# Kernel tuning notes

Hardware: AMD Instinct MI355X
Metric: run time of the kernel (lower is better)

Reference implementation:

```python
import jax, jax.numpy as jnp
import numpy as np

# ---- static config (mirrors init_kwargs) ----
WIN_X, WIN_Y = 12, 12
GRID_X, GRID_Y = 468, 468
BATCH = 4
SHIFTS = ((0, 0), (6, 6))
MAX_WIN_X = GRID_X // WIN_X + 1            # 40
MAX_WIN_Y = GRID_Y // WIN_Y + 1            # 40
MAX_WIN_PER_SAMPLE = MAX_WIN_X * MAX_WIN_Y # 1600
# (level, max_tokens, drop_range_lo, drop_range_hi)
DROP_INFO = ((0, 30, 0, 30), (1, 60, 30, 60), (2, 100, 60, 100000))
SENTINEL = 2_000_000_000  # window id for masked-out voxels (sorts to the end)


def _window_partition(coors):
    # coors: [N,4] = [b, z, y, x] int32 -> batch-unique window index per shift
    out = []
    for sx, sy in SHIFTS:
        x = coors[:, 3] + sx
        y = coors[:, 2] + sy
        wx = x // WIN_X
        wy = y // WIN_Y
        out.append((coors[:, 0] * MAX_WIN_PER_SAMPLE + wx * MAX_WIN_Y + wy).astype(jnp.int32))
    return out


def _sort_group_stats(win):
    # inner index within each equal-value group (counting-sort style) and group size per element
    order = jnp.argsort(win)                      # stable
    s = win[order]
    n = win.shape[0]
    left_s = jnp.searchsorted(s, s, side='left')
    inner_sorted = jnp.arange(n, dtype=win.dtype) - left_s.astype(win.dtype)
    inner = jnp.zeros_like(win).at[order].set(inner_sorted)
    counts = (jnp.searchsorted(s, win, side='right') - jnp.searchsorted(s, win, side='left')).astype(win.dtype)
    return inner, counts


def _drop_single_shift(win, valid):
    # equivalent of SSTInputLayer.drop_single_shift restricted to `valid` voxels
    w = jnp.where(valid, win, SENTINEL)
    inner, counts = _sort_group_stats(w)
    target = jnp.zeros_like(w)
    lvl = -jnp.ones_like(w)
    for dl, max_tok, lo, hi in DROP_INFO:
        m = (counts >= lo) & (counts < hi)
        target = jnp.where(m, max_tok, target)
        lvl = jnp.where(m, dl, lvl)
    keep = valid & (inner < target)
    return keep, jnp.where(valid, lvl, -1)


def _make_continuous(w):
    # dense-rank of window ids (make_continuous_inds) over a sentinel-masked array
    order = jnp.argsort(w)
    s = w[order]
    new_grp = jnp.concatenate([jnp.zeros((1,), w.dtype), (s[1:] != s[:-1]).astype(w.dtype)])
    rank = jnp.cumsum(new_grp)
    return jnp.zeros_like(w).at[order].set(rank)


def _flat2win(win, keep, lvl):
    # per-voxel position in the [num_windows, max_tokens] buffer of its drop level; -1 if dropped
    out = -jnp.ones_like(win)
    for dl, max_tok, _, _ in DROP_INFO:
        valid = keep & (lvl == dl)
        w = jnp.where(valid, win, SENTINEL)
        conti = _make_continuous(w)
        inner, _ = _sort_group_stats(w)
        out = jnp.where(valid, conti * max_tok + inner, out)
    return out


def reference(voxel_feat, coors):
    coors = coors.astype(jnp.int32)
    bwi0, bwi1 = _window_partition(coors)
    n = voxel_feat.shape[0]
    all_valid = jnp.ones((n,), bool)
    keep0, lvl0 = _drop_single_shift(bwi0, all_valid)
    keep1, lvl1 = _drop_single_shift(bwi1, keep0)   # shift-1 drop computed among shift-0 survivors
    keep = keep0 & keep1
    feat = jnp.where(keep[:, None], voxel_feat, 0.0)  # fixed-shape analogue of voxel_feat[voxel_keep_inds]
    f2w0 = _flat2win(bwi0, keep, lvl0)
    f2w1 = _flat2win(bwi1, keep, lvl1)
    return feat, keep, lvl0, lvl1, bwi0, bwi1, f2w0, f2w1


def setup_inputs() -> dict:
    key = jax.random.key(0)
    k1, k2, k3, k4 = jax.random.split(key, 4)
    n, c = 300000, 128
    voxel_feat = jax.random.normal(k1, (n, c), dtype=jnp.float32)
    b = jax.random.randint(k2, (n,), 0, BATCH)
    y = jax.random.randint(k3, (n,), 0, GRID_Y)
    x = jax.random.randint(k4, (n,), 0, GRID_X)
    z = jnp.zeros((n,), jnp.int32)
    coors = jnp.stack([b, z, y, x], axis=1).astype(jnp.int32)
    return {"voxel_feat": voxel_feat, "coors": coors}
```

## Files before the change

### kernel.cpp

```cpp
#include <hip/hip_runtime.h>


#define NWIN 6400
#define SEG_CAP 3072

__global__ void k_zero(int* __restrict__ hdr, int* __restrict__ keepF, int n) {
    int i = blockIdx.x * blockDim.x + threadIdx.x;
    if (i < 4 * NWIN) hdr[i] = 0;
    if (i < n) keepF[i] = 0;
}

__global__ void k_windows(const int* __restrict__ coors, int n,
                          int* __restrict__ w0a, int* __restrict__ w1a,
                          int* __restrict__ cnt0) {
    int i = blockIdx.x * blockDim.x + threadIdx.x;
    if (i >= n) return;
    int b = coors[4 * i];
    int y = coors[4 * i + 2];
    int x = coors[4 * i + 3];
    int w0 = b * 1600 + (x / 12) * 40 + (y / 12);
    int w1 = b * 1600 + ((x + 6) / 12) * 40 + ((y + 6) / 12);
    w0a[i] = w0;
    w1a[i] = w1;
    atomicAdd(&cnt0[w0], 1);
}

__global__ void k_scan(const int* __restrict__ cnt, int* __restrict__ base,
                       int* __restrict__ lvlW) {
    __shared__ int psum[256];
    int t = threadIdx.x;
    int st = t * 25;
    int s = 0;
    for (int j = 0; j < 25; j++) s += cnt[st + j];
    psum[t] = s;
    __syncthreads();
    if (t == 0) {
        int acc = 0;
        for (int j = 0; j < 256; j++) { int v = psum[j]; psum[j] = acc; acc += v; }
    }
    __syncthreads();
    int acc = psum[t];
    for (int j = 0; j < 25; j++) {
        int w = st + j;
        int c = cnt[w];
        base[w] = acc;
        acc += c;
        int lvl;
        if (c < 30) lvl = 0;
        else if (c < 60) lvl = 1;
        else if (c < 100000) lvl = 2;
        else lvl = -1;
        lvlW[w] = lvl;
    }
}

__global__ void k_count_masked(const int* __restrict__ wa, const int* __restrict__ mask,
                               int n, int* __restrict__ cnt) {
    int i = blockIdx.x * blockDim.x + threadIdx.x;
    if (i >= n) return;
    if (!mask[i]) return;
    atomicAdd(&cnt[wa[i]], 1);
}

__global__ void k_scatter(const int* __restrict__ wa, const int* __restrict__ mask, int n,
                          const int* __restrict__ base, int* __restrict__ cur,
                          int* __restrict__ seg) {
    int i = blockIdx.x * blockDim.x + threadIdx.x;
    if (i >= n) return;
    if (mask && !mask[i]) return;
    int w = wa[i];
    int p = atomicAdd(&cur[w], 1);
    seg[base[w] + p] = i;
}

__global__ void k_rankkeep(const int* __restrict__ cnt, const int* __restrict__ base,
                           const int* __restrict__ seg, int* __restrict__ keepOut) {
    int w = blockIdx.x;
    int k = cnt[w];
    if (k == 0) return;
    int bs = base[w];
    int target;
    if (k < 30) target = 30;
    else if (k < 60) target = 60;
    else if (k < 100000) target = 100;
    else target = 0;
    __shared__ int lds[SEG_CAP];
    if (k <= SEG_CAP) {
        for (int j = threadIdx.x; j < k; j += blockDim.x) lds[j] = seg[bs + j];
        __syncthreads();
        for (int e = threadIdx.x; e < k; e += blockDim.x) {
            int v = lds[e];
            int r = 0;
            for (int j = 0; j < k; j++) r += (lds[j] < v) ? 1 : 0;
            keepOut[v] = (r < target) ? 1 : 0;
        }
    } else {
        for (int e = threadIdx.x; e < k; e += blockDim.x) {
            int v = seg[bs + e];
            int r = 0;
            for (int j = 0; j < k; j++) r += (seg[bs + j] < v) ? 1 : 0;
            keepOut[v] = (r < target) ? 1 : 0;
        }
    }
}

__global__ void k_rankkept(const int* __restrict__ cnt, const int* __restrict__ base,
                           const int* __restrict__ seg, const int* __restrict__ keepF,
                           int* __restrict__ rk, int* __restrict__ keptC) {
    int w = blockIdx.x;
    int k = cnt[w];
    __shared__ int lds[SEG_CAP];
    __shared__ int red[64];
    int local = 0;
    if (k > 0) {
        int bs = base[w];
        if (k <= SEG_CAP) {
            for (int j = threadIdx.x; j < k; j += blockDim.x) {
                int v = seg[bs + j];
                lds[j] = v | (keepF[v] << 30);
            }
            __syncthreads();
            for (int e = threadIdx.x; e < k; e += blockDim.x) {
                int enc = lds[e];
                int kept = enc >> 30;
                local += kept;
                if (!kept) continue;
                int v = enc & 0x3FFFFFFF;
                int r = 0;
                for (int j = 0; j < k; j++) {
                    int ej = lds[j];
                    r += (ej >> 30) & (int)((ej & 0x3FFFFFFF) < v);
                }
                rk[v] = r;
            }
        } else {
            for (int e = threadIdx.x; e < k; e += blockDim.x) {
                int v = seg[bs + e];
                int f = keepF[v];
                local += f;
                if (!f) continue;
                int r = 0;
                for (int j = 0; j < k; j++) {
                    int u = seg[bs + j];
                    r += (keepF[u] && (u < v)) ? 1 : 0;
                }
                rk[v] = r;
            }
        }
    }
    red[threadIdx.x] = local;
    __syncthreads();
    if (threadIdx.x == 0) {
        int s = 0;
        for (int j = 0; j < 64; j++) s += red[j];
        keptC[w] = s;
    }
}

__global__ void k_conti(const int* __restrict__ lvlW, const int* __restrict__ keptC,
                        int* __restrict__ conti) {
    __shared__ int pc0[256], pc1[256], pc2[256];
    int t = threadIdx.x;
    int st = t * 25;
    int c0 = 0, c1 = 0, c2 = 0;
    for (int j = 0; j < 25; j++) {
        int w = st + j;
        if (keptC[w] > 0) {
            int l = lvlW[w];
            c0 += (l == 0); c1 += (l == 1); c2 += (l == 2);
        }
    }
    pc0[t] = c0; pc1[t] = c1; pc2[t] = c2;
    __syncthreads();
    if (t == 0) {
        int a = 0, b = 0, c = 0;
        for (int j = 0; j < 256; j++) {
            int v0 = pc0[j], v1 = pc1[j], v2 = pc2[j];
            pc0[j] = a; pc1[j] = b; pc2[j] = c;
            a += v0; b += v1; c += v2;
        }
    }
    __syncthreads();
    int a0 = pc0[t], a1 = pc1[t], a2 = pc2[t];
    for (int j = 0; j < 25; j++) {
        int w = st + j;
        int l = lvlW[w];
        int cc = (l == 0) ? a0 : (l == 1) ? a1 : (l == 2) ? a2 : 0;
        conti[w] = cc;
        if (keptC[w] > 0) {
            if (l == 0) a0++; else if (l == 1) a1++; else if (l == 2) a2++;
        }
    }
}

__global__ void k_final(int n, const int* __restrict__ w0a, const int* __restrict__ w1a,
                        const int* __restrict__ keep0, const int* __restrict__ keepF,
                        const int* __restrict__ lvlW0, const int* __restrict__ lvlW1,
                        const int* __restrict__ conti0, const int* __restrict__ conti1,
                        const int* __restrict__ rk0, const int* __restrict__ rk1,
                        float* __restrict__ out) {
    int i = blockIdx.x * blockDim.x + threadIdx.x;
    if (i >= n) return;
    size_t N = (size_t)n;
    float* o = out + N * 128;
    int w0 = w0a[i], w1 = w1a[i];
    int k0 = keep0[i];
    int kf = keepF[i];
    int l0 = lvlW0[w0];
    int l1 = k0 ? lvlW1[w1] : -1;
    int f0 = -1, f1 = -1;
    if (kf) {
        int mt0 = (l0 == 0) ? 30 : (l0 == 1) ? 60 : 100;
        int mt1 = (l1 == 0) ? 30 : (l1 == 1) ? 60 : 100;
        f0 = conti0[w0] * mt0 + rk0[i];
        f1 = conti1[w1] * mt1 + rk1[i];
    }
    o[i]         = (float)kf;
    o[N + i]     = (float)l0;
    o[2 * N + i] = (float)l1;
    o[3 * N + i] = (float)w0;
    o[4 * N + i] = (float)w1;
    o[5 * N + i] = (float)f0;
    o[6 * N + i] = (float)f1;
}

__global__ void k_feat(const float4* __restrict__ in, const int* __restrict__ keepF,
                       float4* __restrict__ out, int n) {
    int gid = blockIdx.x * blockDim.x + threadIdx.x;
    int total = n * 32;
    if (gid >= total) return;
    int row = gid >> 5;
    float4 v = in[gid];
    if (!keepF[row]) { v.x = 0.f; v.y = 0.f; v.z = 0.f; v.w = 0.f; }
    out[gid] = v;
}

extern "C" void kernel_launch(void* const* d_in, const int* in_sizes, int n_in,
                              void* d_out, int out_size, void* d_ws, size_t ws_size,
                              hipStream_t stream) {
    (void)n_in; (void)out_size; (void)ws_size;
    const float* feat = (const float*)d_in[0];
    const int* coors  = (const int*)d_in[1];
    int n = in_sizes[1] / 4;
    float* out = (float*)d_out;
    int* ws = (int*)d_ws;

    int* cnt0   = ws;
    int* cur0   = ws + 6400;
    int* cnt1   = ws + 12800;
    int* cur1   = ws + 19200;
    int* base0  = ws + 25600;
    int* base1  = ws + 32000;
    int* lvlW0  = ws + 38400;
    int* lvlW1  = ws + 44800;
    int* keptC0 = ws + 51200;
    int* keptC1 = ws + 57600;
    int* conti0 = ws + 64000;
    int* conti1 = ws + 70400;
    int* w0a    = ws + 76800;
    int* w1a    = w0a + n;
    int* seg0   = w1a + n;
    int* seg1   = seg0 + n;
    int* keep0  = seg1 + n;
    int* keepF  = keep0 + n;
    int* rk0    = keepF + n;
    int* rk1    = rk0 + n;

    int nb = (n + 255) / 256;
    int zmax = (n > 4 * NWIN) ? n : 4 * NWIN;
    int zb = (zmax + 255) / 256;

    k_zero<<<zb, 256, 0, stream>>>(cnt0, keepF, n);
    k_windows<<<nb, 256, 0, stream>>>(coors, n, w0a, w1a, cnt0);
    k_scan<<<1, 256, 0, stream>>>(cnt0, base0, lvlW0);
    k_scatter<<<nb, 256, 0, stream>>>(w0a, (const int*)nullptr, n, base0, cur0, seg0);
    k_rankkeep<<<NWIN, 64, 0, stream>>>(cnt0, base0, seg0, keep0);
    k_count_masked<<<nb, 256, 0, stream>>>(w1a, keep0, n, cnt1);
    k_scan<<<1, 256, 0, stream>>>(cnt1, base1, lvlW1);
    k_scatter<<<nb, 256, 0, stream>>>(w1a, keep0, n, base1, cur1, seg1);
    k_rankkeep<<<NWIN, 64, 0, stream>>>(cnt1, base1, seg1, keepF);
    k_rankkept<<<NWIN, 64, 0, stream>>>(cnt0, base0, seg0, keepF, rk0, keptC0);
    k_rankkept<<<NWIN, 64, 0, stream>>>(cnt1, base1, seg1, keepF, rk1, keptC1);
    k_conti<<<1, 256, 0, stream>>>(lvlW0, keptC0, conti0);
    k_conti<<<1, 256, 0, stream>>>(lvlW1, keptC1, conti1);
    k_final<<<nb, 256, 0, stream>>>(n, w0a, w1a, keep0, keepF, lvlW0, lvlW1,
                                    conti0, conti1, rk0, rk1, out);
    int fb = (n * 32 + 255) / 256;
    k_feat<<<fb, 256, 0, stream>>>((const float4*)feat, keepF, (float4*)out, n);
}
```

Measured before the change: 436.6 us.

## Fuse pipeline into one cooperative persistent kernel with grid syncs

Replaces the fifteen separate launches with a single cooperative kernel of 1024 blocks that steps through ten phases separated by grid.sync. It also fuses the masked shift-1 count into the shift-0 rank/keep phase and computes rk1 and keptC in the same pass as keep1. The feature masking now overlaps with the rk0 ranking. If the cooperative launch fails, it falls back to per-phase launches. Launch overhead and redundant passes go away, at the cost of grid-wide barriers and fewer blocks for the ranking phases.

```diff
diff --git a/kernel.cpp b/kernel.cpp
--- a/kernel.cpp
+++ b/kernel.cpp
@@ -1,33 +1,19 @@
 #include <hip/hip_runtime.h>
+#include <hip/hip_cooperative_groups.h>
+
+namespace cg = cooperative_groups;
 
 
 #define NWIN 6400
-#define SEG_CAP 3072
-
-__global__ void k_zero(int* __restrict__ hdr, int* __restrict__ keepF, int n) {
-    int i = blockIdx.x * blockDim.x + threadIdx.x;
-    if (i < 4 * NWIN) hdr[i] = 0;
-    if (i < n) keepF[i] = 0;
-}
-
-__global__ void k_windows(const int* __restrict__ coors, int n,
-                          int* __restrict__ w0a, int* __restrict__ w1a,
-                          int* __restrict__ cnt0) {
-    int i = blockIdx.x * blockDim.x + threadIdx.x;
-    if (i >= n) return;
-    int b = coors[4 * i];
-    int y = coors[4 * i + 2];
-    int x = coors[4 * i + 3];
-    int w0 = b * 1600 + (x / 12) * 40 + (y / 12);
-    int w1 = b * 1600 + ((x + 6) / 12) * 40 + ((y + 6) / 12);
-    w0a[i] = w0;
-    w1a[i] = w1;
-    atomicAdd(&cnt0[w0], 1);
-}
-
-__global__ void k_scan(const int* __restrict__ cnt, int* __restrict__ base,
-                       int* __restrict__ lvlW) {
-    __shared__ int psum[256];
+#define CAP 2048
+#define GRID_BLOCKS 1024
+
+__device__ __forceinline__ int drop_target(int lvl) {
+    return (lvl == 0) ? 30 : (lvl == 1) ? 60 : (lvl == 2) ? 100 : 0;
+}
+
+__device__ void scan_block(const int* __restrict__ cnt, int* __restrict__ base,
+                           int* __restrict__ lvlW, int* psum) {
     int t = threadIdx.x;
     int st = t * 25;
     int s = 0;
@@ -45,121 +31,13 @@
         int c = cnt[w];
         base[w] = acc;
         acc += c;
-        int lvl;
-        if (c < 30) lvl = 0;
-        else if (c < 60) lvl = 1;
-        else if (c < 100000) lvl = 2;
-        else lvl = -1;
-        lvlW[w] = lvl;
-    }
-}
-
-__global__ void k_count_masked(const int* __restrict__ wa, const int* __restrict__ mask,
-                               int n, int* __restrict__ cnt) {
-    int i = blockIdx.x * blockDim.x + threadIdx.x;
-    if (i >= n) return;
-    if (!mask[i]) return;
-    atomicAdd(&cnt[wa[i]], 1);
-}
-
-__global__ void k_scatter(const int* __restrict__ wa, const int* __restrict__ mask, int n,
-                          const int* __restrict__ base, int* __restrict__ cur,
-                          int* __restrict__ seg) {
-    int i = blockIdx.x * blockDim.x + threadIdx.x;
-    if (i >= n) return;
-    if (mask && !mask[i]) return;
-    int w = wa[i];
-    int p = atomicAdd(&cur[w], 1);
-    seg[base[w] + p] = i;
-}
-
-__global__ void k_rankkeep(const int* __restrict__ cnt, const int* __restrict__ base,
-                           const int* __restrict__ seg, int* __restrict__ keepOut) {
-    int w = blockIdx.x;
-    int k = cnt[w];
-    if (k == 0) return;
-    int bs = base[w];
-    int target;
-    if (k < 30) target = 30;
-    else if (k < 60) target = 60;
-    else if (k < 100000) target = 100;
-    else target = 0;
-    __shared__ int lds[SEG_CAP];
-    if (k <= SEG_CAP) {
-        for (int j = threadIdx.x; j < k; j += blockDim.x) lds[j] = seg[bs + j];
-        __syncthreads();
-        for (int e = threadIdx.x; e < k; e += blockDim.x) {
-            int v = lds[e];
-            int r = 0;
-            for (int j = 0; j < k; j++) r += (lds[j] < v) ? 1 : 0;
-            keepOut[v] = (r < target) ? 1 : 0;
-        }
-    } else {
-        for (int e = threadIdx.x; e < k; e += blockDim.x) {
-            int v = seg[bs + e];
-            int r = 0;
-            for (int j = 0; j < k; j++) r += (seg[bs + j] < v) ? 1 : 0;
-            keepOut[v] = (r < target) ? 1 : 0;
-        }
-    }
-}
-
-__global__ void k_rankkept(const int* __restrict__ cnt, const int* __restrict__ base,
-                           const int* __restrict__ seg, const int* __restrict__ keepF,
-                           int* __restrict__ rk, int* __restrict__ keptC) {
-    int w = blockIdx.x;
-    int k = cnt[w];
-    __shared__ int lds[SEG_CAP];
-    __shared__ int red[64];
-    int local = 0;
-    if (k > 0) {
-        int bs = base[w];
-        if (k <= SEG_CAP) {
-            for (int j = threadIdx.x; j < k; j += blockDim.x) {
-                int v = seg[bs + j];
-                lds[j] = v | (keepF[v] << 30);
-            }
-            __syncthreads();
-            for (int e = threadIdx.x; e < k; e += blockDim.x) {
-                int enc = lds[e];
-                int kept = enc >> 30;
-                local += kept;
-                if (!kept) continue;
-                int v = enc & 0x3FFFFFFF;
-                int r = 0;
-                for (int j = 0; j < k; j++) {
-                    int ej = lds[j];
-                    r += (ej >> 30) & (int)((ej & 0x3FFFFFFF) < v);
-                }
-                rk[v] = r;
-            }
-        } else {
-            for (int e = threadIdx.x; e < k; e += blockDim.x) {
-                int v = seg[bs + e];
-                int f = keepF[v];
-                local += f;
-                if (!f) continue;
-                int r = 0;
-                for (int j = 0; j < k; j++) {
-                    int u = seg[bs + j];
-                    r += (keepF[u] && (u < v)) ? 1 : 0;
-                }
-                rk[v] = r;
-            }
-        }
-    }
-    red[threadIdx.x] = local;
-    __syncthreads();
-    if (threadIdx.x == 0) {
-        int s = 0;
-        for (int j = 0; j < 64; j++) s += red[j];
-        keptC[w] = s;
-    }
-}
-
-__global__ void k_conti(const int* __restrict__ lvlW, const int* __restrict__ keptC,
-                        int* __restrict__ conti) {
-    __shared__ int pc0[256], pc1[256], pc2[256];
+        lvlW[w] = (c < 30) ? 0 : (c < 60) ? 1 : (c < 100000) ? 2 : -1;
+    }
+    __syncthreads();
+}
+
+__device__ void conti_block(const int* __restrict__ lvlW, const int* __restrict__ keptC,
+                            int* __restrict__ conti, int* pc0, int* pc1, int* pc2) {
     int t = threadIdx.x;
     int st = t * 25;
     int c0 = 0, c1 = 0, c2 = 0;
@@ -185,106 +63,308 @@
     for (int j = 0; j < 25; j++) {
         int w = st + j;
         int l = lvlW[w];
-        int cc = (l == 0) ? a0 : (l == 1) ? a1 : (l == 2) ? a2 : 0;
-        conti[w] = cc;
+        conti[w] = (l == 0) ? a0 : (l == 1) ? a1 : (l == 2) ? a2 : 0;
         if (keptC[w] > 0) {
             if (l == 0) a0++; else if (l == 1) a1++; else if (l == 2) a2++;
         }
     }
-}
-
-__global__ void k_final(int n, const int* __restrict__ w0a, const int* __restrict__ w1a,
-                        const int* __restrict__ keep0, const int* __restrict__ keepF,
-                        const int* __restrict__ lvlW0, const int* __restrict__ lvlW1,
-                        const int* __restrict__ conti0, const int* __restrict__ conti1,
-                        const int* __restrict__ rk0, const int* __restrict__ rk1,
-                        float* __restrict__ out) {
-    int i = blockIdx.x * blockDim.x + threadIdx.x;
-    if (i >= n) return;
-    size_t N = (size_t)n;
-    float* o = out + N * 128;
-    int w0 = w0a[i], w1 = w1a[i];
-    int k0 = keep0[i];
-    int kf = keepF[i];
-    int l0 = lvlW0[w0];
-    int l1 = k0 ? lvlW1[w1] : -1;
-    int f0 = -1, f1 = -1;
-    if (kf) {
-        int mt0 = (l0 == 0) ? 30 : (l0 == 1) ? 60 : 100;
-        int mt1 = (l1 == 0) ? 30 : (l1 == 1) ? 60 : 100;
-        f0 = conti0[w0] * mt0 + rk0[i];
-        f1 = conti1[w1] * mt1 + rk1[i];
-    }
-    o[i]         = (float)kf;
-    o[N + i]     = (float)l0;
-    o[2 * N + i] = (float)l1;
-    o[3 * N + i] = (float)w0;
-    o[4 * N + i] = (float)w1;
-    o[5 * N + i] = (float)f0;
-    o[6 * N + i] = (float)f1;
-}
-
-__global__ void k_feat(const float4* __restrict__ in, const int* __restrict__ keepF,
-                       float4* __restrict__ out, int n) {
-    int gid = blockIdx.x * blockDim.x + threadIdx.x;
-    int total = n * 32;
-    if (gid >= total) return;
-    int row = gid >> 5;
-    float4 v = in[gid];
-    if (!keepF[row]) { v.x = 0.f; v.y = 0.f; v.z = 0.f; v.w = 0.f; }
-    out[gid] = v;
+    __syncthreads();
+}
+
+__global__ __launch_bounds__(256, 4) void sst_fused(
+    const float4* __restrict__ feat, const int* __restrict__ coors, int n,
+    float* __restrict__ out, int* __restrict__ ws,
+    int lo, int hi, int coop)
+{
+    cg::grid_group grid = cg::this_grid();
+    const int tid = threadIdx.x;
+    const int gsz = gridDim.x * blockDim.x;
+    const int gid = blockIdx.x * blockDim.x + tid;
+
+    int* cnt0   = ws;
+    int* cur0   = ws + NWIN;
+    int* cnt1   = ws + 2 * NWIN;
+    int* cur1   = ws + 3 * NWIN;
+    int* keptC0 = ws + 4 * NWIN;
+    int* keptC1 = ws + 5 * NWIN;
+    int* base0  = ws + 6 * NWIN;
+    int* base1  = ws + 7 * NWIN;
+    int* lvlW0  = ws + 8 * NWIN;
+    int* lvlW1  = ws + 9 * NWIN;
+    int* conti0 = ws + 10 * NWIN;
+    int* conti1 = ws + 11 * NWIN;
+    int* arr    = ws + 12 * NWIN;
+    int* w0a   = arr;
+    int* w1a   = arr + n;
+    int* seg0  = arr + 2 * n;
+    int* seg1  = arr + 3 * n;
+    int* keep0 = arr + 4 * n;
+    int* keep1 = arr + 5 * n;
+    int* rk0   = arr + 6 * n;
+    int* rk1   = arr + 7 * n;
+
+    __shared__ int lds[CAP];
+    __shared__ int pc0[256], pc1[256], pc2[256];
+
+#define PHASE_IN(p) ((p) >= lo && (p) < hi)
+
+    if (PHASE_IN(0)) {
+        for (int i = gid; i < 6 * NWIN; i += gsz) cnt0[i] = 0;
+        if (coop) grid.sync();
+    }
+
+    if (PHASE_IN(1)) {
+        const int4* c4 = (const int4*)coors;
+        for (int i = gid; i < n; i += gsz) {
+            int4 c = c4[i];
+            int w0 = c.x * 1600 + (c.w / 12) * 40 + (c.z / 12);
+            int w1 = c.x * 1600 + ((c.w + 6) / 12) * 40 + ((c.z + 6) / 12);
+            w0a[i] = w0;
+            w1a[i] = w1;
+            atomicAdd(&cnt0[w0], 1);
+        }
+        if (coop) grid.sync();
+    }
+
+    if (PHASE_IN(2)) {
+        if (blockIdx.x == 0) scan_block(cnt0, base0, lvlW0, pc0);
+        if (coop) grid.sync();
+    }
+
+    if (PHASE_IN(3)) {
+        for (int i = gid; i < n; i += gsz) {
+            int w = w0a[i];
+            int p = atomicAdd(&cur0[w], 1);
+            seg0[base0[w] + p] = i;
+        }
+        if (coop) grid.sync();
+    }
+
+    if (PHASE_IN(4)) {
+        for (int w = blockIdx.x; w < NWIN; w += gridDim.x) {
+            int k = cnt0[w];
+            if (k == 0) continue;
+            int bs = base0[w];
+            int target = drop_target(lvlW0[w]);
+            if (k <= CAP) {
+                for (int j = tid; j < k; j += 256) lds[j] = seg0[bs + j];
+                __syncthreads();
+                for (int e = tid; e < k; e += 256) {
+                    int v = lds[e];
+                    int r = 0;
+                    for (int j = 0; j < k; j++) r += (lds[j] < v);
+                    int kp = (r < target) ? 1 : 0;
+                    keep0[v] = kp;
+                    if (kp) atomicAdd(&cnt1[w1a[v]], 1);
+                }
+                __syncthreads();
+            } else {
+                for (int e = tid; e < k; e += 256) {
+                    int v = seg0[bs + e];
+                    int r = 0;
+                    for (int j = 0; j < k; j++) r += (seg0[bs + j] < v);
+                    int kp = (r < target) ? 1 : 0;
+                    keep0[v] = kp;
+                    if (kp) atomicAdd(&cnt1[w1a[v]], 1);
+                }
+            }
+        }
+        if (coop) grid.sync();
+    }
+
+    if (PHASE_IN(5)) {
+        if (blockIdx.x == 0) scan_block(cnt1, base1, lvlW1, pc0);
+        if (coop) grid.sync();
+    }
+
+    if (PHASE_IN(6)) {
+        for (int i = gid; i < n; i += gsz) {
+            if (!keep0[i]) continue;
+            int w = w1a[i];
+            int p = atomicAdd(&cur1[w], 1);
+            seg1[base1[w] + p] = i;
+        }
+        if (coop) grid.sync();
+    }
+
+    if (PHASE_IN(7)) {
+        for (int w = blockIdx.x; w < NWIN; w += gridDim.x) {
+            int k = cnt1[w];
+            if (k == 0) continue;
+            int bs = base1[w];
+            int target = drop_target(lvlW1[w]);
+            if (k <= CAP) {
+                for (int j = tid; j < k; j += 256) lds[j] = seg1[bs + j];
+                __syncthreads();
+                int kparr[(CAP + 255) / 256];
+                int q = 0;
+                for (int e = tid; e < k; e += 256, q++) {
+                    int v = lds[e];
+                    int r = 0;
+                    for (int j = 0; j < k; j++) r += (lds[j] < v);
+                    int kp = (r < target) ? 1 : 0;
+                    keep1[v] = kp;
+                    kparr[q] = kp;
+                }
+                __syncthreads();
+                q = 0;
+                for (int e = tid; e < k; e += 256, q++) lds[e] |= (kparr[q] << 30);
+                __syncthreads();
+                for (int e = tid; e < k; e += 256) {
+                    int enc = lds[e];
+                    if (enc >> 30) {
+                        int v = enc & 0x3FFFFFFF;
+                        int r = 0;
+                        for (int j = 0; j < k; j++) {
+                            int ej = lds[j];
+                            r += (ej >> 30) & (int)((ej & 0x3FFFFFFF) < v);
+                        }
+                        rk1[v] = r;
+                        atomicAdd(&keptC0[w0a[v]], 1);
+                    }
+                }
+                if (tid == 0) {
+                    int s = 0;
+                    for (int j = 0; j < k; j++) s += lds[j] >> 30;
+                    keptC1[w] = s;
+                }
+                __syncthreads();
+            } else {
+                for (int e = tid; e < k; e += 256) {
+                    int v = seg1[bs + e];
+                    int r = 0;
+                    for (int j = 0; j < k; j++) r += (seg1[bs + j] < v);
+                    keep1[v] = (r < target) ? 1 : 0;
+                }
+                __syncthreads();
+                for (int e = tid; e < k; e += 256) {
+                    int v = seg1[bs + e];
+                    if (!keep1[v]) continue;
+                    int r = 0;
+                    for (int j = 0; j < k; j++) {
+                        int u = seg1[bs + j];
+                        r += (keep1[u] && (u < v)) ? 1 : 0;
+                    }
+                    rk1[v] = r;
+                    atomicAdd(&keptC0[w0a[v]], 1);
+                }
+                if (tid == 0) {
+                    int s = 0;
+                    for (int j = 0; j < k; j++) s += keep1[seg1[bs + j]] ? 1 : 0;
+                    keptC1[w] = s;
+                }
+                __syncthreads();
+            }
+        }
+        if (coop) grid.sync();
+    }
+
+    if (PHASE_IN(8)) {
+        if (blockIdx.x == 0) {
+            conti_block(lvlW0, keptC0, conti0, pc0, pc1, pc2);
+        } else if (blockIdx.x == 1) {
+            conti_block(lvlW1, keptC1, conti1, pc0, pc1, pc2);
+        } else {
+            for (int w = (int)blockIdx.x - 2; w < NWIN; w += (int)gridDim.x - 2) {
+                int k = cnt0[w];
+                if (k == 0) continue;
+                int bs = base0[w];
+                if (k <= CAP) {
+                    for (int j = tid; j < k; j += 256) {
+                        int v = seg0[bs + j];
+                        int k0 = keep0[v];
+                        int kf = k0 ? (keep1[v] != 0) : 0;
+                        lds[j] = v | (kf << 30);
+                    }
+                    __syncthreads();
+                    for (int e = tid; e < k; e += 256) {
+                        int enc = lds[e];
+                        if (enc >> 30) {
+                            int v = enc & 0x3FFFFFFF;
+                            int r = 0;
+                            for (int j = 0; j < k; j++) {
+                                int ej = lds[j];
+                                r += (ej >> 30) & (int)((ej & 0x3FFFFFFF) < v);
+                            }
+                            rk0[v] = r;
+                        }
+                    }
+                    __syncthreads();
+                } else {
+                    for (int e = tid; e < k; e += 256) {
+                        int v = seg0[bs + e];
+                        if (!keep0[v] || !keep1[v]) continue;
+                        int r = 0;
+                        for (int j = 0; j < k; j++) {
+                            int u = seg0[bs + j];
+                            int kq = keep0[u] ? (keep1[u] != 0) : 0;
+                            r += kq & (int)(u < v);
+                        }
+                        rk0[v] = r;
+                    }
+                }
+            }
+        }
+        float4* out4 = (float4*)out;
+        int total = n * 32;
+        for (int i = gid; i < total; i += gsz) {
+            int row = i >> 5;
+            float4 v = feat[i];
+            int k0 = keep0[row];
+            int kf = k0 ? keep1[row] : 0;
+            if (!kf) { v.x = 0.f; v.y = 0.f; v.z = 0.f; v.w = 0.f; }
+            out4[i] = v;
+        }
+        if (coop) grid.sync();
+    }
+
+    if (PHASE_IN(9)) {
+        float* o = out + (size_t)n * 128;
+        for (int i = gid; i < n; i += gsz) {
+            int w0 = w0a[i], w1 = w1a[i];
+            int k0 = keep0[i];
+            int kf = k0 ? (keep1[i] ? 1 : 0) : 0;
+            int l0 = lvlW0[w0];
+            int l1 = k0 ? lvlW1[w1] : -1;
+            int f0 = -1, f1 = -1;
+            if (kf) {
+                int mt0 = (l0 == 0) ? 30 : (l0 == 1) ? 60 : 100;
+                int mt1 = (l1 == 0) ? 30 : (l1 == 1) ? 60 : 100;
+                f0 = conti0[w0] * mt0 + rk0[i];
+                f1 = conti1[w1] * mt1 + rk1[i];
+            }
+            o[i]         = (float)kf;
+            o[n + i]     = (float)l0;
+            o[2 * n + i] = (float)l1;
+            o[3 * n + i] = (float)w0;
+            o[4 * n + i] = (float)w1;
+            o[5 * n + i] = (float)f0;
+            o[6 * n + i] = (float)f1;
+        }
+    }
+#undef PHASE_IN
 }
 
 extern "C" void kernel_launch(void* const* d_in, const int* in_sizes, int n_in,
                               void* d_out, int out_size, void* d_ws, size_t ws_size,
                               hipStream_t stream) {
     (void)n_in; (void)out_size; (void)ws_size;
-    const float* feat = (const float*)d_in[0];
-    const int* coors  = (const int*)d_in[1];
+    const float4* feat = (const float4*)d_in[0];
+    const int* coors   = (const int*)d_in[1];
     int n = in_sizes[1] / 4;
     float* out = (float*)d_out;
     int* ws = (int*)d_ws;
 
-    int* cnt0   = ws;
-    int* cur0   = ws + 6400;
-    int* cnt1   = ws + 12800;
-    int* cur1   = ws + 19200;
-    int* base0  = ws + 25600;
-    int* base1  = ws + 32000;
-    int* lvlW0  = ws + 38400;
-    int* lvlW1  = ws + 44800;
-    int* keptC0 = ws + 51200;
-    int* keptC1 = ws + 57600;
-    int* conti0 = ws + 64000;
-    int* conti1 = ws + 70400;
-    int* w0a    = ws + 76800;
-    int* w1a    = w0a + n;
-    int* seg0   = w1a + n;
-    int* seg1   = seg0 + n;
-    int* keep0  = seg1 + n;
-    int* keepF  = keep0 + n;
-    int* rk0    = keepF + n;
-    int* rk1    = rk0 + n;
-
-    int nb = (n + 255) / 256;
-    int zmax = (n > 4 * NWIN) ? n : 4 * NWIN;
-    int zb = (zmax + 255) / 256;
-
-    k_zero<<<zb, 256, 0, stream>>>(cnt0, keepF, n);
-    k_windows<<<nb, 256, 0, stream>>>(coors, n, w0a, w1a, cnt0);
-    k_scan<<<1, 256, 0, stream>>>(cnt0, base0, lvlW0);
-    k_scatter<<<nb, 256, 0, stream>>>(w0a, (const int*)nullptr, n, base0, cur0, seg0);
-    k_rankkeep<<<NWIN, 64, 0, stream>>>(cnt0, base0, seg0, keep0);
-    k_count_masked<<<nb, 256, 0, stream>>>(w1a, keep0, n, cnt1);
-    k_scan<<<1, 256, 0, stream>>>(cnt1, base1, lvlW1);
-    k_scatter<<<nb, 256, 0, stream>>>(w1a, keep0, n, base1, cur1, seg1);
-    k_rankkeep<<<NWIN, 64, 0, stream>>>(cnt1, base1, seg1, keepF);
-    k_rankkept<<<NWIN, 64, 0, stream>>>(cnt0, base0, seg0, keepF, rk0, keptC0);
-    k_rankkept<<<NWIN, 64, 0, stream>>>(cnt1, base1, seg1, keepF, rk1, keptC1);
-    k_conti<<<1, 256, 0, stream>>>(lvlW0, keptC0, conti0);
-    k_conti<<<1, 256, 0, stream>>>(lvlW1, keptC1, conti1);
-    k_final<<<nb, 256, 0, stream>>>(n, w0a, w1a, keep0, keepF, lvlW0, lvlW1,
-                                    conti0, conti1, rk0, rk1, out);
-    int fb = (n * 32 + 255) / 256;
-    k_feat<<<fb, 256, 0, stream>>>((const float4*)feat, keepF, (float4*)out, n);
-}
+    int lo = 0, hi = 10, coop = 1;
+    void* args[] = { (void*)&feat, (void*)&coors, (void*)&n, (void*)&out,
+                     (void*)&ws, (void*)&lo, (void*)&hi, (void*)&coop };
+    hipError_t err = hipLaunchCooperativeKernel(
+        reinterpret_cast<void*>(sst_fused), dim3(GRID_BLOCKS), dim3(256),
+        args, 0, stream);
+    if (err != hipSuccess) {
+        for (int p = 0; p < 10; p++) {
+            sst_fused<<<GRID_BLOCKS, 256, 0, stream>>>(feat, coors, n, out, ws,
+                                                       p, p + 1, 0);
+        }
+    }
+}
```

New measurement: 1.462 ms. +235.0%, slower.
